# Performance work log

Measured on AMD Instinct MI355X. Metric: run time of the kernel, lower is better.

Reference implementation:

```python
import jax, jax.numpy as jnp
import numpy as np

N_NODES = 100000
N_EDGES = 1600000
D_IN, D_HID, D_OUT = 64, 64, 32


def _glorot(key, shape):
    fan_in = shape[0]
    return jax.random.normal(key, shape, dtype=jnp.float32) / np.sqrt(fan_in)


def setup_inputs() -> dict:
    key = jax.random.key(0)
    ks = jax.random.split(key, 12)
    x = jax.random.normal(ks[0], (N_NODES, D_IN), dtype=jnp.float32)
    edge_index = jax.random.randint(ks[1], (2, N_EDGES), 0, N_NODES, dtype=jnp.int32)
    dims = [(D_IN, D_HID), (D_HID, D_HID), (D_HID, D_OUT)]
    params = {}
    for i, (din, dout) in enumerate(dims):
        params[f"Wl{i}"] = _glorot(ks[2 + 3 * i], (din, dout))
        params[f"Wr{i}"] = _glorot(ks[3 + 3 * i], (din, dout))
        params[f"b{i}"] = jnp.zeros((dout,), dtype=jnp.float32)
    return {"x": x, "edge_index": edge_index, **params}


def _sage_conv(h, src, dst, deg_inv, Wl, Wr, b):
    # mean-aggregate neighbor features: gather from src, scatter-sum to dst
    msg_sum = jax.ops.segment_sum(h[src], dst, num_segments=N_NODES)  # [N, F]
    mean = msg_sum * deg_inv[:, None]
    # lin_l(mean) + bias + lin_r(h)  (PyG SAGEConv: bias lives in lin_l)
    return mean @ Wl + b + h @ Wr


def reference(x, edge_index, Wl0, Wr0, b0, Wl1, Wr1, b1, Wl2, Wr2, b2):
    src, dst = edge_index[0], edge_index[1]
    deg = jax.ops.segment_sum(jnp.ones((N_EDGES,), x.dtype), dst, num_segments=N_NODES)
    deg_inv = 1.0 / jnp.maximum(deg, 1.0)  # mean with clamp for isolated nodes
    h = jax.nn.elu(_sage_conv(x, src, dst, deg_inv, Wl0, Wr0, b0))
    h = jax.nn.elu(_sage_conv(h, src, dst, deg_inv, Wl1, Wr1, b1))
    return _sage_conv(h, src, dst, deg_inv, Wl2, Wr2, b2)
```

## Files before the change

### kernel.cpp

```cpp
#include <hip/hip_runtime.h>
#include <cstdint>
#include <cstddef>


constexpr int SBW = 256;
constexpr int LOGSBW = 8;
constexpr int CAPS = 4608;
constexpr int CHK = 2048;

typedef __attribute__((ext_vector_type(8))) short s16x8;
typedef __attribute__((ext_vector_type(4))) float f32x4;

__device__ inline unsigned short f2bf(float f) {
  unsigned u = __builtin_bit_cast(unsigned, f);
  u += 0x7FFFu + ((u >> 16) & 1u);
  return (unsigned short)(u >> 16);
}
__device__ inline float bf2f(unsigned short b) {
  unsigned u = ((unsigned)b) << 16;
  return __builtin_bit_cast(float, u);
}


__global__ __launch_bounds__(256) void bin_coarse(const int* __restrict__ src,
                                                  const int* __restrict__ dst,
                                                  int* __restrict__ bcur,
                                                  unsigned int* __restrict__ coarse,
                                                  int NSB, int E) {
  __shared__ int h[512];
  __shared__ unsigned ed[CHK];
  __shared__ short sb[CHK];
  const int tid = threadIdx.x;
  for (int i = tid; i < NSB; i += 256) h[i] = 0;
  __syncthreads();
  const int e0 = blockIdx.x * CHK;
  const int e1 = min(E, e0 + CHK);
  for (int e = e0 + tid; e < e1; e += 256) {
    int d = dst[e];
    int s = src[e];
    int b = d >> LOGSBW;
    ed[e - e0] = (unsigned)s | ((unsigned)(d & (SBW - 1)) << 17);
    sb[e - e0] = (short)b;
    atomicAdd(&h[b], 1);
  }
  __syncthreads();
  for (int i = tid; i < NSB; i += 256) {
    int c = h[i];
    h[i] = c ? (i * CAPS + atomicAdd(&bcur[i], c)) : 0;
  }
  __syncthreads();
  const int n = e1 - e0;
  for (int k = tid; k < n; k += 256) {
    int b = sb[k];
    int pos = atomicAdd(&h[b], 1);
    if (pos < (b + 1) * CAPS)
      coarse[pos] = ed[k];
  }
}


__global__ __launch_bounds__(256) void super_csr(const unsigned int* __restrict__ coarse,
                                                 const int* __restrict__ bcur,
                                                 int* __restrict__ rowstart,
                                                 int* __restrict__ degarr,
                                                 float* __restrict__ deg_inv,
                                                 int* __restrict__ colidx,
                                                 int N) {
  __shared__ int cnt[SBW];
  __shared__ int sc[SBW];
  __shared__ int cur[SBW];
  const int b = blockIdx.x;
  const int tid = threadIdx.x;
  cnt[tid] = 0;
  __syncthreads();
  const int ec = min(bcur[b], CAPS);
  const int base = b * CAPS;
  for (int e = tid; e < ec; e += 256)
    atomicAdd(&cnt[coarse[base + e] >> 17], 1);
  __syncthreads();
  int v = cnt[tid];
  sc[tid] = v;
  __syncthreads();
  for (int off = 1; off < SBW; off <<= 1) {
    int y = sc[tid];
    if (tid >= off) y += sc[tid - off];
    __syncthreads();
    sc[tid] = y;
    __syncthreads();
  }
  int ex = sc[tid] - v;
  cur[tid] = ex;
  int gn = b * SBW + tid;
  if (gn < N) {
    rowstart[gn] = base + ex;
    degarr[gn] = v;
    deg_inv[gn] = 1.0f / (float)(v > 1 ? v : 1);
  }
  __syncthreads();
  for (int e = tid; e < ec; e += 256) {
    unsigned p = coarse[base + e];
    int dl = (int)(p >> 17);
    int s = (int)(p & 0x1FFFFu);
    int l = atomicAdd(&cur[dl], 1);
    colidx[base + l] = s;
  }
}


__global__ __launch_bounds__(256) void gemm0_mfma(const float* __restrict__ x,
                                                  const float* __restrict__ Wl,
                                                  const float* __restrict__ Wr,
                                                  const float* __restrict__ bias,
                                                  unsigned short* __restrict__ t_out,
                                                  float* __restrict__ r_out, int N) {
  constexpr int DOUT = 64;
  constexpr int NTT = DOUT / 16;
  constexpr int SK = 72;
  __shared__ short Wt[2 * DOUT * SK];

  const int tid = threadIdx.x;
  for (int idx = tid; idx < 64 * DOUT; idx += 256) {
    int k = idx / DOUT, c = idx % DOUT;
    Wt[c * SK + k] = (short)f2bf(Wl[idx]);
    Wt[(c + DOUT) * SK + k] = (short)f2bf(Wr[idx]);
  }
  __syncthreads();

  const int wv = tid >> 6, lane = tid & 63;
  const int q = lane >> 4, m = lane & 15;
  const int row = blockIdx.x * 64 + wv * 16 + m;
  const int rowc = row < N ? row : N - 1;
  const float* xp = &x[(size_t)rowc * 64];
  float4 f0 = *(const float4*)&xp[q * 8];
  float4 f1 = *(const float4*)&xp[q * 8 + 4];
  float4 f2 = *(const float4*)&xp[32 + q * 8];
  float4 f3 = *(const float4*)&xp[32 + q * 8 + 4];
  s16x8 a0, a1;
  a0[0] = (short)f2bf(f0.x); a0[1] = (short)f2bf(f0.y);
  a0[2] = (short)f2bf(f0.z); a0[3] = (short)f2bf(f0.w);
  a0[4] = (short)f2bf(f1.x); a0[5] = (short)f2bf(f1.y);
  a0[6] = (short)f2bf(f1.z); a0[7] = (short)f2bf(f1.w);
  a1[0] = (short)f2bf(f2.x); a1[1] = (short)f2bf(f2.y);
  a1[2] = (short)f2bf(f2.z); a1[3] = (short)f2bf(f2.w);
  a1[4] = (short)f2bf(f3.x); a1[5] = (short)f2bf(f3.y);
  a1[6] = (short)f2bf(f3.z); a1[7] = (short)f2bf(f3.w);

  f32x4 acc[2 * NTT];
#pragma unroll
  for (int c = 0; c < 2 * NTT; ++c) acc[c] = (f32x4){0.f, 0.f, 0.f, 0.f};
#pragma unroll
  for (int c = 0; c < 2 * NTT; ++c) {
    const short* wp = &Wt[(c * 16 + m) * SK];
    s16x8 b0 = *(const s16x8*)&wp[q * 8];
    s16x8 b1 = *(const s16x8*)&wp[32 + q * 8];
    acc[c] = __builtin_amdgcn_mfma_f32_16x16x32_bf16(a0, b0, acc[c], 0, 0, 0);
    acc[c] = __builtin_amdgcn_mfma_f32_16x16x32_bf16(a1, b1, acc[c], 0, 0, 0);
  }

  const int orow = blockIdx.x * 64 + wv * 16 + q * 4;
#pragma unroll
  for (int c = 0; c < NTT; ++c) {
#pragma unroll
    for (int i = 0; i < 4; ++i) {
      int r_ = orow + i;
      if (r_ < N) t_out[(size_t)r_ * DOUT + c * 16 + m] = f2bf(acc[c][i]);
    }
  }
#pragma unroll
  for (int c = 0; c < NTT; ++c) {
    float bv = bias[c * 16 + m];
#pragma unroll
    for (int i = 0; i < 4; ++i) {
      int r_ = orow + i;
      if (r_ < N) r_out[(size_t)r_ * DOUT + c * 16 + m] = acc[NTT + c][i] + bv;
    }
  }
}


template <int DOUT>
__global__ __launch_bounds__(256) void fused_gather_gemm(
    const uint2* __restrict__ t_in, const float* __restrict__ r_in,
    const float* __restrict__ deg_inv, const int* __restrict__ rowstart,
    const int* __restrict__ degarr, const int* __restrict__ colidx,
    const float* __restrict__ Wl, const float* __restrict__ Wr,
    const float* __restrict__ bias,
    unsigned short* __restrict__ t_out, float* __restrict__ r_out, int N) {
  constexpr int NTT = DOUT / 16;
  constexpr int SK = 72;
  __shared__ short Wt[2 * DOUT * SK];
  __shared__ short hs[64 * SK];

  const int tid = threadIdx.x;
  for (int idx = tid; idx < 64 * DOUT; idx += 256) {
    int k = idx / DOUT, c = idx % DOUT;
    Wt[c * SK + k] = (short)f2bf(Wl[idx]);
    Wt[(c + DOUT) * SK + k] = (short)f2bf(Wr[idx]);
  }

  const int sg = tid >> 4, lane = tid & 15;
  const int node0 = blockIdx.x * 64;
#pragma unroll
  for (int p = 0; p < 4; ++p) {
    int nl = p * 16 + sg;
    int node = node0 + nl;
    if (node < N) {
      int b = rowstart[node];
      int e = b + degarr[node];
      float s0 = 0.f, s1 = 0.f, s2 = 0.f, s3 = 0.f;
      int i = b;
      for (; i + 8 <= e; i += 8) {
        uint2 v[8];
#pragma unroll
        for (int j = 0; j < 8; ++j)
          v[j] = t_in[(size_t)colidx[i + j] * 16 + lane];
#pragma unroll
        for (int j = 0; j < 8; ++j) {
          s0 += bf2f((unsigned short)(v[j].x & 0xFFFFu));
          s1 += bf2f((unsigned short)(v[j].x >> 16));
          s2 += bf2f((unsigned short)(v[j].y & 0xFFFFu));
          s3 += bf2f((unsigned short)(v[j].y >> 16));
        }
      }
      for (; i < e; ++i) {
        uint2 v = t_in[(size_t)colidx[i] * 16 + lane];
        s0 += bf2f((unsigned short)(v.x & 0xFFFFu));
        s1 += bf2f((unsigned short)(v.x >> 16));
        s2 += bf2f((unsigned short)(v.y & 0xFFFFu));
        s3 += bf2f((unsigned short)(v.y >> 16));
      }
      float dv = deg_inv[node];
      float4 rv = *(const float4*)&r_in[(size_t)node * 64 + 4 * lane];
      float a0 = s0 * dv + rv.x;
      float a1 = s1 * dv + rv.y;
      float a2 = s2 * dv + rv.z;
      float a3 = s3 * dv + rv.w;
      a0 = a0 > 0.f ? a0 : (expf(a0) - 1.f);
      a1 = a1 > 0.f ? a1 : (expf(a1) - 1.f);
      a2 = a2 > 0.f ? a2 : (expf(a2) - 1.f);
      a3 = a3 > 0.f ? a3 : (expf(a3) - 1.f);
      ushort4 hv;
      hv.x = f2bf(a0); hv.y = f2bf(a1); hv.z = f2bf(a2); hv.w = f2bf(a3);
      *(ushort4*)&hs[nl * SK + 4 * lane] = hv;
    }
  }
  __syncthreads();

  const int wv = tid >> 6, l64 = tid & 63;
  const int q = l64 >> 4, m = l64 & 15;
  const s16x8 a0 = *(const s16x8*)&hs[(wv * 16 + m) * SK + q * 8];
  const s16x8 a1 = *(const s16x8*)&hs[(wv * 16 + m) * SK + 32 + q * 8];

  f32x4 acc[2 * NTT];
#pragma unroll
  for (int c = 0; c < 2 * NTT; ++c) acc[c] = (f32x4){0.f, 0.f, 0.f, 0.f};
#pragma unroll
  for (int c = 0; c < 2 * NTT; ++c) {
    const short* wp = &Wt[(c * 16 + m) * SK];
    s16x8 b0 = *(const s16x8*)&wp[q * 8];
    s16x8 b1 = *(const s16x8*)&wp[32 + q * 8];
    acc[c] = __builtin_amdgcn_mfma_f32_16x16x32_bf16(a0, b0, acc[c], 0, 0, 0);
    acc[c] = __builtin_amdgcn_mfma_f32_16x16x32_bf16(a1, b1, acc[c], 0, 0, 0);
  }

  const int orow = blockIdx.x * 64 + wv * 16 + q * 4;
#pragma unroll
  for (int c = 0; c < NTT; ++c) {
#pragma unroll
    for (int i = 0; i < 4; ++i) {
      int r_ = orow + i;
      if (r_ < N) t_out[(size_t)r_ * DOUT + c * 16 + m] = f2bf(acc[c][i]);
    }
  }
#pragma unroll
  for (int c = 0; c < NTT; ++c) {
    float bv = bias[c * 16 + m];
#pragma unroll
    for (int i = 0; i < 4; ++i) {
      int r_ = orow + i;
      if (r_ < N) r_out[(size_t)r_ * DOUT + c * 16 + m] = acc[NTT + c][i] + bv;
    }
  }
}


__global__ __launch_bounds__(256) void gather_out(const uint2* __restrict__ t,
                                                  const float* __restrict__ r,
                                                  const float* __restrict__ deg_inv,
                                                  const int* __restrict__ rowstart,
                                                  const int* __restrict__ degarr,
                                                  const int* __restrict__ colidx,
                                                  float* __restrict__ out, int N) {
  constexpr int L = 8;
  int node = blockIdx.x * 32 + threadIdx.x / L;
  int lane = threadIdx.x & (L - 1);
  if (node >= N) return;
  int b = rowstart[node];
  int e = b + degarr[node];
  float s0 = 0.f, s1 = 0.f, s2 = 0.f, s3 = 0.f;
  int i = b;
  for (; i + 8 <= e; i += 8) {
    uint2 v[8];
#pragma unroll
    for (int j = 0; j < 8; ++j)
      v[j] = t[(size_t)colidx[i + j] * L + lane];
#pragma unroll
    for (int j = 0; j < 8; ++j) {
      s0 += bf2f((unsigned short)(v[j].x & 0xFFFFu));
      s1 += bf2f((unsigned short)(v[j].x >> 16));
      s2 += bf2f((unsigned short)(v[j].y & 0xFFFFu));
      s3 += bf2f((unsigned short)(v[j].y >> 16));
    }
  }
  for (; i < e; ++i) {
    uint2 v = t[(size_t)colidx[i] * L + lane];
    s0 += bf2f((unsigned short)(v.x & 0xFFFFu));
    s1 += bf2f((unsigned short)(v.x >> 16));
    s2 += bf2f((unsigned short)(v.y & 0xFFFFu));
    s3 += bf2f((unsigned short)(v.y >> 16));
  }
  float dv = deg_inv[node];
  float4 rv = *(const float4*)&r[(size_t)node * 32 + 4 * lane];
  *(float4*)&out[(size_t)node * 32 + 4 * lane] =
      make_float4(s0 * dv + rv.x, s1 * dv + rv.y, s2 * dv + rv.z, s3 * dv + rv.w);
}


extern "C" void kernel_launch(void* const* d_in, const int* in_sizes, int n_in,
                              void* d_out, int out_size, void* d_ws, size_t ws_size,
                              hipStream_t stream) {
  const float* x   = (const float*)d_in[0];
  const int*   ei  = (const int*)d_in[1];
  const float* Wl0 = (const float*)d_in[2];
  const float* Wr0 = (const float*)d_in[3];
  const float* b0  = (const float*)d_in[4];
  const float* Wl1 = (const float*)d_in[5];
  const float* Wr1 = (const float*)d_in[6];
  const float* b1  = (const float*)d_in[7];
  const float* Wl2 = (const float*)d_in[8];
  const float* Wr2 = (const float*)d_in[9];
  const float* b2  = (const float*)d_in[10];
  float* out = (float*)d_out;

  const int N = in_sizes[0] / 64;
  const int E = in_sizes[1] / 2;
  const int* srcv = ei;
  const int* dstv = ei + E;
  const int NSB = (N + SBW - 1) >> LOGSBW;

  auto al = [](size_t v) { return (v + 255) & ~(size_t)255; };
  char* w = (char*)d_ws;
  size_t oBcur = 0;
  size_t oRow  = oBcur + al(4 * (size_t)NSB);
  size_t oDeg  = oRow + al(4 * (size_t)N);
  size_t oDinv = oDeg + al(4 * (size_t)N);
  size_t oBin  = oDinv + al(4 * (size_t)N);
  size_t oCol  = oBin + al(4 * (size_t)NSB * CAPS);
  size_t oP0   = oCol + al(4 * (size_t)NSB * CAPS);
  size_t oP1   = oP0 + al(2 * (size_t)N * 64);
  size_t oR0   = oP1 + al(2 * (size_t)N * 64);
  size_t oR1   = oR0 + al(4 * (size_t)N * 64);

  int*            bcur     = (int*)(w + oBcur);
  int*            rowstart = (int*)(w + oRow);
  int*            degarr   = (int*)(w + oDeg);
  float*          deg_inv  = (float*)(w + oDinv);
  unsigned*       coarse   = (unsigned*)(w + oBin);
  int*            colidx   = (int*)(w + oCol);
  unsigned short* P0       = (unsigned short*)(w + oP0);
  unsigned short* P1       = (unsigned short*)(w + oP1);
  float*          R0       = (float*)(w + oR0);
  float*          R1       = (float*)(w + oR1);

  hipMemsetAsync(bcur, 0, (size_t)NSB * 4, stream);

  int bbl = (E + CHK - 1) / CHK;
  bin_coarse<<<bbl, 256, 0, stream>>>(srcv, dstv, bcur, coarse, NSB, E);
  super_csr<<<NSB, 256, 0, stream>>>(coarse, bcur, rowstart, degarr, deg_inv, colidx, N);

  int gb = (N + 63) / 64;
  gemm0_mfma<<<gb, 256, 0, stream>>>(x, Wl0, Wr0, b0, P0, R0, N);
  fused_gather_gemm<64><<<gb, 256, 0, stream>>>(
      (const uint2*)P0, R0, deg_inv, rowstart, degarr, colidx,
      Wl1, Wr1, b1, P1, R1, N);
  fused_gather_gemm<32><<<gb, 256, 0, stream>>>(
      (const uint2*)P1, R1, deg_inv, rowstart, degarr, colidx,
      Wl2, Wr2, b2, P0, R0, N);
  gather_out<<<(N + 31) / 32, 256, 0, stream>>>(
      (const uint2*)P0, R0, deg_inv, rowstart, degarr, colidx, out, N);
}
```

Baseline: 294.5 us.

## Store gathered 64-wide projections in FP8 and split gather from GEMM

Layer-0 and layer-1 neighbor projections are now written as FP8 instead of BF16, which halves the bytes moved in the random-access gather for those two layers. The fused gather+GEMM kernel is split into a separate gather kernel (8 lanes per node, ELU, BF16 output to an intermediate buffer) and a plain MFMA GEMM kernel. Weight staging is rewritten to pack two BF16 values per shared-memory store. The split adds one extra round trip of the intermediate activations through global memory and two more launches, and FP8 storage lowers the accuracy of the messages.

```diff
diff --git a/kernel.cpp b/kernel.cpp
--- a/kernel.cpp
+++ b/kernel.cpp
@@ -10,6 +10,7 @@
 
 typedef __attribute__((ext_vector_type(8))) short s16x8;
 typedef __attribute__((ext_vector_type(4))) float f32x4;
+typedef __attribute__((ext_vector_type(2))) float f32x2;
 
 __device__ inline unsigned short f2bf(float f) {
   unsigned u = __builtin_bit_cast(unsigned, f);
@@ -19,6 +20,10 @@
 __device__ inline float bf2f(unsigned short b) {
   unsigned u = ((unsigned)b) << 16;
   return __builtin_bit_cast(float, u);
+}
+__device__ inline unsigned char f2fp8(float f) {
+  int p = __builtin_amdgcn_cvt_pk_fp8_f32(f, f, 0, false);
+  return (unsigned char)(p & 0xFF);
 }
 
 
@@ -107,23 +112,34 @@
 }
 
 
+template <int DOUT, int SK>
+__device__ inline void stage_weights(short* Wt, const float* __restrict__ Wl,
+                                     const float* __restrict__ Wr, int tid) {
+  for (int idx = tid; idx < DOUT * 32; idx += 256) {
+    int c = idx >> 5;
+    int k2 = (idx & 31) << 1;
+    unsigned l0 = f2bf(Wl[k2 * DOUT + c]);
+    unsigned l1 = f2bf(Wl[(k2 + 1) * DOUT + c]);
+    *(unsigned*)&Wt[c * SK + k2] = l0 | (l1 << 16);
+    unsigned r0 = f2bf(Wr[k2 * DOUT + c]);
+    unsigned r1 = f2bf(Wr[(k2 + 1) * DOUT + c]);
+    *(unsigned*)&Wt[(c + DOUT) * SK + k2] = r0 | (r1 << 16);
+  }
+}
+
+
 __global__ __launch_bounds__(256) void gemm0_mfma(const float* __restrict__ x,
                                                   const float* __restrict__ Wl,
                                                   const float* __restrict__ Wr,
                                                   const float* __restrict__ bias,
-                                                  unsigned short* __restrict__ t_out,
+                                                  unsigned char* __restrict__ t_out,
                                                   float* __restrict__ r_out, int N) {
   constexpr int DOUT = 64;
-  constexpr int NTT = DOUT / 16;
+  constexpr int NTT = 4;
   constexpr int SK = 72;
   __shared__ short Wt[2 * DOUT * SK];
-
   const int tid = threadIdx.x;
-  for (int idx = tid; idx < 64 * DOUT; idx += 256) {
-    int k = idx / DOUT, c = idx % DOUT;
-    Wt[c * SK + k] = (short)f2bf(Wl[idx]);
-    Wt[(c + DOUT) * SK + k] = (short)f2bf(Wr[idx]);
-  }
+  stage_weights<DOUT, SK>(Wt, Wl, Wr, tid);
   __syncthreads();
 
   const int wv = tid >> 6, lane = tid & 63;
@@ -163,7 +179,7 @@
 #pragma unroll
     for (int i = 0; i < 4; ++i) {
       int r_ = orow + i;
-      if (r_ < N) t_out[(size_t)r_ * DOUT + c * 16 + m] = f2bf(acc[c][i]);
+      if (r_ < N) t_out[(size_t)r_ * DOUT + c * 16 + m] = f2fp8(acc[c][i]);
     }
   }
 #pragma unroll
@@ -178,78 +194,26 @@
 }
 
 
-template <int DOUT>
-__global__ __launch_bounds__(256) void fused_gather_gemm(
-    const uint2* __restrict__ t_in, const float* __restrict__ r_in,
-    const float* __restrict__ deg_inv, const int* __restrict__ rowstart,
-    const int* __restrict__ degarr, const int* __restrict__ colidx,
-    const float* __restrict__ Wl, const float* __restrict__ Wr,
-    const float* __restrict__ bias,
-    unsigned short* __restrict__ t_out, float* __restrict__ r_out, int N) {
+template <int DOUT, bool TFP8>
+__global__ __launch_bounds__(256) void gemm_mfma(const unsigned short* __restrict__ Hm,
+                                                 const float* __restrict__ Wl,
+                                                 const float* __restrict__ Wr,
+                                                 const float* __restrict__ bias,
+                                                 void* __restrict__ t_out,
+                                                 float* __restrict__ r_out, int N) {
   constexpr int NTT = DOUT / 16;
   constexpr int SK = 72;
   __shared__ short Wt[2 * DOUT * SK];
-  __shared__ short hs[64 * SK];
-
   const int tid = threadIdx.x;
-  for (int idx = tid; idx < 64 * DOUT; idx += 256) {
-    int k = idx / DOUT, c = idx % DOUT;
-    Wt[c * SK + k] = (short)f2bf(Wl[idx]);
-    Wt[(c + DOUT) * SK + k] = (short)f2bf(Wr[idx]);
-  }
-
-  const int sg = tid >> 4, lane = tid & 15;
-  const int node0 = blockIdx.x * 64;
-#pragma unroll
-  for (int p = 0; p < 4; ++p) {
-    int nl = p * 16 + sg;
-    int node = node0 + nl;
-    if (node < N) {
-      int b = rowstart[node];
-      int e = b + degarr[node];
-      float s0 = 0.f, s1 = 0.f, s2 = 0.f, s3 = 0.f;
-      int i = b;
-      for (; i + 8 <= e; i += 8) {
-        uint2 v[8];
-#pragma unroll
-        for (int j = 0; j < 8; ++j)
-          v[j] = t_in[(size_t)colidx[i + j] * 16 + lane];
-#pragma unroll
-        for (int j = 0; j < 8; ++j) {
-          s0 += bf2f((unsigned short)(v[j].x & 0xFFFFu));
-          s1 += bf2f((unsigned short)(v[j].x >> 16));
-          s2 += bf2f((unsigned short)(v[j].y & 0xFFFFu));
-          s3 += bf2f((unsigned short)(v[j].y >> 16));
-        }
-      }
-      for (; i < e; ++i) {
-        uint2 v = t_in[(size_t)colidx[i] * 16 + lane];
-        s0 += bf2f((unsigned short)(v.x & 0xFFFFu));
-        s1 += bf2f((unsigned short)(v.x >> 16));
-        s2 += bf2f((unsigned short)(v.y & 0xFFFFu));
-        s3 += bf2f((unsigned short)(v.y >> 16));
-      }
-      float dv = deg_inv[node];
-      float4 rv = *(const float4*)&r_in[(size_t)node * 64 + 4 * lane];
-      float a0 = s0 * dv + rv.x;
-      float a1 = s1 * dv + rv.y;
-      float a2 = s2 * dv + rv.z;
-      float a3 = s3 * dv + rv.w;
-      a0 = a0 > 0.f ? a0 : (expf(a0) - 1.f);
-      a1 = a1 > 0.f ? a1 : (expf(a1) - 1.f);
-      a2 = a2 > 0.f ? a2 : (expf(a2) - 1.f);
-      a3 = a3 > 0.f ? a3 : (expf(a3) - 1.f);
-      ushort4 hv;
-      hv.x = f2bf(a0); hv.y = f2bf(a1); hv.z = f2bf(a2); hv.w = f2bf(a3);
-      *(ushort4*)&hs[nl * SK + 4 * lane] = hv;
-    }
-  }
-  __syncthreads();
-
-  const int wv = tid >> 6, l64 = tid & 63;
-  const int q = l64 >> 4, m = l64 & 15;
-  const s16x8 a0 = *(const s16x8*)&hs[(wv * 16 + m) * SK + q * 8];
-  const s16x8 a1 = *(const s16x8*)&hs[(wv * 16 + m) * SK + 32 + q * 8];
+  stage_weights<DOUT, SK>(Wt, Wl, Wr, tid);
+  __syncthreads();
+
+  const int wv = tid >> 6, lane = tid & 63;
+  const int q = lane >> 4, m = lane & 15;
+  const int row = blockIdx.x * 64 + wv * 16 + m;
+  const int rowc = row < N ? row : N - 1;
+  const s16x8 a0 = *(const s16x8*)&Hm[(size_t)rowc * 64 + q * 8];
+  const s16x8 a1 = *(const s16x8*)&Hm[(size_t)rowc * 64 + 32 + q * 8];
 
   f32x4 acc[2 * NTT];
 #pragma unroll
@@ -269,7 +233,12 @@
 #pragma unroll
     for (int i = 0; i < 4; ++i) {
       int r_ = orow + i;
-      if (r_ < N) t_out[(size_t)r_ * DOUT + c * 16 + m] = f2bf(acc[c][i]);
+      if (r_ < N) {
+        if (TFP8)
+          ((unsigned char*)t_out)[(size_t)r_ * DOUT + c * 16 + m] = f2fp8(acc[c][i]);
+        else
+          ((unsigned short*)t_out)[(size_t)r_ * DOUT + c * 16 + m] = f2bf(acc[c][i]);
+      }
     }
   }
 #pragma unroll
@@ -281,6 +250,66 @@
       if (r_ < N) r_out[(size_t)r_ * DOUT + c * 16 + m] = acc[NTT + c][i] + bv;
     }
   }
+}
+
+
+__global__ __launch_bounds__(256) void gather_fp8(const uint2* __restrict__ t,
+                                                  const float* __restrict__ r,
+                                                  const float* __restrict__ deg_inv,
+                                                  const int* __restrict__ rowstart,
+                                                  const int* __restrict__ degarr,
+                                                  const int* __restrict__ colidx,
+                                                  unsigned short* __restrict__ Xout,
+                                                  int N) {
+  int node = blockIdx.x * 32 + (threadIdx.x >> 3);
+  int lane = threadIdx.x & 7;
+  if (node >= N) return;
+  int b = rowstart[node];
+  int e = b + degarr[node];
+  float s[8];
+#pragma unroll
+  for (int k = 0; k < 8; ++k) s[k] = 0.f;
+  int i = b;
+  for (; i + 8 <= e; i += 8) {
+    uint2 v[8];
+#pragma unroll
+    for (int j = 0; j < 8; ++j)
+      v[j] = t[(size_t)colidx[i + j] * 8 + lane];
+#pragma unroll
+    for (int j = 0; j < 8; ++j) {
+      f32x2 p0 = __builtin_amdgcn_cvt_pk_f32_fp8((int)v[j].x, false);
+      f32x2 p1 = __builtin_amdgcn_cvt_pk_f32_fp8((int)v[j].x, true);
+      f32x2 p2 = __builtin_amdgcn_cvt_pk_f32_fp8((int)v[j].y, false);
+      f32x2 p3 = __builtin_amdgcn_cvt_pk_f32_fp8((int)v[j].y, true);
+      s[0] += p0[0]; s[1] += p0[1]; s[2] += p1[0]; s[3] += p1[1];
+      s[4] += p2[0]; s[5] += p2[1]; s[6] += p3[0]; s[7] += p3[1];
+    }
+  }
+  for (; i < e; ++i) {
+    uint2 v = t[(size_t)colidx[i] * 8 + lane];
+    f32x2 p0 = __builtin_amdgcn_cvt_pk_f32_fp8((int)v.x, false);
+    f32x2 p1 = __builtin_amdgcn_cvt_pk_f32_fp8((int)v.x, true);
+    f32x2 p2 = __builtin_amdgcn_cvt_pk_f32_fp8((int)v.y, false);
+    f32x2 p3 = __builtin_amdgcn_cvt_pk_f32_fp8((int)v.y, true);
+    s[0] += p0[0]; s[1] += p0[1]; s[2] += p1[0]; s[3] += p1[1];
+    s[4] += p2[0]; s[5] += p2[1]; s[6] += p3[0]; s[7] += p3[1];
+  }
+  float dv = deg_inv[node];
+  const float* rp = &r[(size_t)node * 64 + lane * 8];
+  float4 r0 = *(const float4*)&rp[0];
+  float4 r1 = *(const float4*)&rp[4];
+  float a[8];
+  a[0] = s[0] * dv + r0.x; a[1] = s[1] * dv + r0.y;
+  a[2] = s[2] * dv + r0.z; a[3] = s[3] * dv + r0.w;
+  a[4] = s[4] * dv + r1.x; a[5] = s[5] * dv + r1.y;
+  a[6] = s[6] * dv + r1.z; a[7] = s[7] * dv + r1.w;
+  s16x8 hv;
+#pragma unroll
+  for (int k = 0; k < 8; ++k) {
+    float ak = a[k] > 0.f ? a[k] : (expf(a[k]) - 1.f);
+    hv[k] = (short)f2bf(ak);
+  }
+  *(s16x8*)&Xout[(size_t)node * 64 + lane * 8] = hv;
 }
 
 
@@ -356,10 +385,10 @@
   size_t oDinv = oDeg + al(4 * (size_t)N);
   size_t oBin  = oDinv + al(4 * (size_t)N);
   size_t oCol  = oBin + al(4 * (size_t)NSB * CAPS);
-  size_t oP0   = oCol + al(4 * (size_t)NSB * CAPS);
-  size_t oP1   = oP0 + al(2 * (size_t)N * 64);
-  size_t oR0   = oP1 + al(2 * (size_t)N * 64);
-  size_t oR1   = oR0 + al(4 * (size_t)N * 64);
+  size_t oP8   = oCol + al(4 * (size_t)NSB * CAPS);
+  size_t oP16  = oP8 + al((size_t)N * 64);
+  size_t oX    = oP16 + al(2 * (size_t)N * 32);
+  size_t oR    = oX + al(2 * (size_t)N * 64);
 
   int*            bcur     = (int*)(w + oBcur);
   int*            rowstart = (int*)(w + oRow);
@@ -367,10 +396,10 @@
   float*          deg_inv  = (float*)(w + oDinv);
   unsigned*       coarse   = (unsigned*)(w + oBin);
   int*            colidx   = (int*)(w + oCol);
-  unsigned short* P0       = (unsigned short*)(w + oP0);
-  unsigned short* P1       = (unsigned short*)(w + oP1);
-  float*          R0       = (float*)(w + oR0);
-  float*          R1       = (float*)(w + oR1);
+  unsigned char*  P8       = (unsigned char*)(w + oP8);
+  unsigned short* P16      = (unsigned short*)(w + oP16);
+  unsigned short* X        = (unsigned short*)(w + oX);
+  float*          R        = (float*)(w + oR);
 
   hipMemsetAsync(bcur, 0, (size_t)NSB * 4, stream);
 
@@ -379,13 +408,14 @@
   super_csr<<<NSB, 256, 0, stream>>>(coarse, bcur, rowstart, degarr, deg_inv, colidx, N);
 
   int gb = (N + 63) / 64;
-  gemm0_mfma<<<gb, 256, 0, stream>>>(x, Wl0, Wr0, b0, P0, R0, N);
-  fused_gather_gemm<64><<<gb, 256, 0, stream>>>(
-      (const uint2*)P0, R0, deg_inv, rowstart, degarr, colidx,
-      Wl1, Wr1, b1, P1, R1, N);
-  fused_gather_gemm<32><<<gb, 256, 0, stream>>>(
-      (const uint2*)P1, R1, deg_inv, rowstart, degarr, colidx,
-      Wl2, Wr2, b2, P0, R0, N);
-  gather_out<<<(N + 31) / 32, 256, 0, stream>>>(
-      (const uint2*)P0, R0, deg_inv, rowstart, degarr, colidx, out, N);
-}
+  int ggb = (N + 31) / 32;
+  gemm0_mfma<<<gb, 256, 0, stream>>>(x, Wl0, Wr0, b0, P8, R, N);
+  gather_fp8<<<ggb, 256, 0, stream>>>((const uint2*)P8, R, deg_inv, rowstart,
+                                      degarr, colidx, X, N);
+  gemm_mfma<64, true><<<gb, 256, 0, stream>>>(X, Wl1, Wr1, b1, P8, R, N);
+  gather_fp8<<<ggb, 256, 0, stream>>>((const uint2*)P8, R, deg_inv, rowstart,
+                                      degarr, colidx, X, N);
+  gemm_mfma<32, false><<<gb, 256, 0, stream>>>(X, Wl2, Wr2, b2, P16, R, N);
+  gather_out<<<ggb, 256, 0, stream>>>((const uint2*)P16, R, deg_inv, rowstart,
+                                      degarr, colidx, out, N);
+}
```

Measured after the change: 316.4 us. +7.5%, slower.
